# Performance work log

Measured on AMD Instinct MI355X. Metric: run time of the kernel, lower is better.

Reference implementation:

```python
import jax, jax.numpy as jnp
import numpy as np

NUM_HEADS = 8
NUM_GROUPS = 32
EPS = 1e-5


def setup_inputs() -> dict:
    key = jax.random.key(0)
    ks = jax.random.split(key, 3)
    B, C, H, W = 8, 512, 32, 32
    X = jax.random.normal(ks[0], (B, C, H, W), dtype=jnp.float32)
    norm_w = jnp.ones((C,), jnp.float32)
    norm_b = jnp.zeros((C,), jnp.float32)
    qkv_w = jax.random.normal(ks[1], (3 * C, C), dtype=jnp.float32) * (1.0 / np.sqrt(C))
    qkv_b = jnp.zeros((3 * C,), jnp.float32)
    proj_w = jax.random.normal(ks[2], (C, C), dtype=jnp.float32) * (1.0 / np.sqrt(C))
    proj_b = jnp.zeros((C,), jnp.float32)
    return {"X": X, "norm_w": norm_w, "norm_b": norm_b,
            "qkv_w": qkv_w, "qkv_b": qkv_b, "proj_w": proj_w, "proj_b": proj_b}


def group_norm(x, w, b):
    B, C, H, W = x.shape
    xg = x.reshape(B, NUM_GROUPS, C // NUM_GROUPS, H, W)
    mean = xg.mean(axis=(2, 3, 4), keepdims=True)
    var = xg.var(axis=(2, 3, 4), keepdims=True)
    xg = (xg - mean) * jax.lax.rsqrt(var + EPS)
    x = xg.reshape(B, C, H, W)
    return x * w[None, :, None, None] + b[None, :, None, None]


def reference(X, norm_w, norm_b, qkv_w, qkv_b, proj_w, proj_b):
    B, C, H, W = X.shape
    hd = C // NUM_HEADS  # head_dim
    residual = X
    Xn = group_norm(X, norm_w, norm_b)
    # 1x1 conv == channel matmul: [B, 3C, H, W]
    qkv = jnp.einsum('oc,bchw->bohw', qkv_w, Xn) + qkv_b[None, :, None, None]
    q, k, v = jnp.split(qkv, 3, axis=1)
    S = H * W
    q = q.reshape(B, NUM_HEADS, hd, S)
    k = k.reshape(B, NUM_HEADS, hd, S)
    v = v.reshape(B, NUM_HEADS, hd, S)
    scale = hd ** -0.5
    attn = jnp.einsum('bhdq,bhdk->bhqk', q, k) * scale  # [B,H,S,S]
    attn = jax.nn.softmax(attn, axis=-1)
    out = jnp.einsum('bhqk,bhdk->bhqd', attn, v)  # [B,H,S,hd]
    out = out.transpose(0, 1, 3, 2).reshape(B, C, H, W)
    out = jnp.einsum('oc,bchw->bohw', proj_w, out) + proj_b[None, :, None, None]
    return out + residual
```

## Files before the change

### kernel.cpp

```cpp
#include <hip/hip_runtime.h>
#include <hip/hip_bf16.h>


#define BATCH 8
#define C 512
#define S 1024
#define HEADS 8
#define OC3 1536

typedef short bf16x8 __attribute__((ext_vector_type(8)));
typedef float f32x4 __attribute__((ext_vector_type(4)));
typedef unsigned u32x2 __attribute__((ext_vector_type(2)));
typedef unsigned short u16;
typedef unsigned short u16x4 __attribute__((ext_vector_type(4)));

__device__ inline short f2bf(float x) {
    union { float f; unsigned u; } v; v.f = x;
    unsigned r = v.u + 0x7fffu + ((v.u >> 16) & 1u);
    return (short)(r >> 16);
}

__device__ inline unsigned cvt_pk_bf16(float lo, float hi) {
    unsigned r;
    asm("v_cvt_pk_bf16_f32 %0, %1, %2" : "=v"(r) : "v"(lo), "v"(hi));
    return r;
}

__device__ inline void gload_lds16(const u16* g, short* l) {
    __builtin_amdgcn_global_load_lds(
        (const __attribute__((address_space(1))) unsigned int*)g,
        (__attribute__((address_space(3))) unsigned int*)l, 16, 0, 0);
}

__global__ __launch_bounds__(512) void prep_kernel(
    const float* __restrict__ X, const float* __restrict__ nw,
    const float* __restrict__ nb, u16* __restrict__ Xn_t,
    const float* __restrict__ wq, const float* __restrict__ wp,
    u16* __restrict__ oq, u16* __restrict__ op)
{
    const int tid = threadIdx.x;
    if (blockIdx.x >= 256) {
        int j = (blockIdx.x - 256) * 512 + tid;
        const float* w; u16* o;
        if (j < 98304) { w = wq; o = oq; }
        else           { w = wp; o = op; j -= 98304; }
        f32x4 a = *(const f32x4*)(w + (size_t)j * 8);
        f32x4 b = *(const f32x4*)(w + (size_t)j * 8 + 4);
        bf16x8 r;
        #pragma unroll
        for (int k = 0; k < 4; ++k) { r[k] = f2bf(a[k]); r[4 + k] = f2bf(b[k]); }
        *(bf16x8*)(o + (size_t)j * 8) = r;
        return;
    }
    const int blk = blockIdx.x;
    const int bi = blk >> 5, g = blk & 31;
    __shared__ __attribute__((aligned(16))) float T[16][1032];
    __shared__ float red[16];
    __shared__ float sh_mr[2];

    const float* Xg = X + ((size_t)bi * C + g * 16) * S;
    float s = 0.f, ss = 0.f;
    #pragma unroll
    for (int r = 0; r < 8; ++r) {
        int idx4 = r * 512 + tid;
        f32x4 v = *(const f32x4*)(Xg + (size_t)idx4 * 4);
        int c = idx4 >> 8, sp = (idx4 * 4) & 1023;
        *(f32x4*)&T[c][sp] = v;
        s  += v[0] + v[1] + v[2] + v[3];
        ss += v[0]*v[0] + v[1]*v[1] + v[2]*v[2] + v[3]*v[3];
    }
    #pragma unroll
    for (int m = 1; m <= 32; m <<= 1) {
        s += __shfl_xor(s, m); ss += __shfl_xor(ss, m);
    }
    if ((tid & 63) == 0) { red[tid >> 6] = s; red[8 + (tid >> 6)] = ss; }
    __syncthreads();
    if (tid == 0) {
        float S1 = 0.f, S2 = 0.f;
        #pragma unroll
        for (int w = 0; w < 8; ++w) { S1 += red[w]; S2 += red[8 + w]; }
        float mean = S1 * (1.f / 16384.f);
        float var  = S2 * (1.f / 16384.f) - mean * mean;
        sh_mr[0] = mean; sh_mr[1] = rsqrtf(var + 1e-5f);
    }
    __syncthreads();
    const float mean = sh_mr[0], rstd = sh_mr[1];
    float rw[16], sb[16];
    #pragma unroll
    for (int c = 0; c < 16; ++c) {
        float w = nw[g * 16 + c], b = nb[g * 16 + c];
        rw[c] = rstd * w;
        sb[c] = b - mean * rw[c];
    }
    #pragma unroll
    for (int r = 0; r < 2; ++r) {
        int sp = r * 512 + tid;
        bf16x8 o0, o1;
        #pragma unroll
        for (int c = 0; c < 8; ++c) o0[c] = f2bf(T[c][sp] * rw[c] + sb[c]);
        #pragma unroll
        for (int c = 0; c < 8; ++c) o1[c] = f2bf(T[8 + c][sp] * rw[8 + c] + sb[8 + c]);
        u16* dst = Xn_t + ((size_t)bi * S + sp) * C + g * 16;
        *(bf16x8*)dst = o0;
        *(bf16x8*)(dst + 8) = o1;
    }
}

__global__ __launch_bounds__(512) void qkv_mfma(
    const u16* __restrict__ A, const u16* __restrict__ Bt,
    const float* __restrict__ bias,
    u16* __restrict__ Qt, u16* __restrict__ Kt, u16* __restrict__ Vn)
{
    const int n0 = blockIdx.x * 256, m0 = blockIdx.y * 256;
    const int bi = blockIdx.z;
    const int tid = threadIdx.x, wave = tid >> 6, lane = tid & 63;
    const int lr = lane & 15, lg = lane >> 4;
    const int wr = wave >> 2, wc = wave & 3;

    __shared__ __attribute__((aligned(16))) short SM[65536];

    f32x4 acc[8][4];
    #pragma unroll
    for (int i = 0; i < 8; ++i)
        #pragma unroll
        for (int j = 0; j < 4; ++j) acc[i][j] = (f32x4){0.f, 0.f, 0.f, 0.f};

    const int l8 = lane >> 3;
    const int c16 = (lane & 7) ^ l8;
    const u16* aBase = A + (size_t)(m0 + wave * 32 + l8) * C + c16 * 8;
    const u16* bBase = Bt + (size_t)bi * S * C + (size_t)(n0 + wave * 32 + l8) * C + c16 * 8;

    auto STAGE = [&](int buf, int t) {
        const int k0 = t * 64;
        short* as = SM + buf * 16384 + wave * 2048;
        short* bs = SM + 32768 + buf * 16384 + wave * 2048;
        #pragma unroll
        for (int j = 0; j < 4; ++j) {
            gload_lds16(aBase + k0 + (size_t)j * 8 * C, as + j * 512);
            gload_lds16(bBase + k0 + (size_t)j * 8 * C, bs + j * 512);
        }
    };

    STAGE(0, 0);
    asm volatile("s_waitcnt vmcnt(0)" ::: "memory");
    __builtin_amdgcn_s_barrier();
    __builtin_amdgcn_sched_barrier(0);

    #pragma unroll
    for (int kt = 0; kt < 8; ++kt) {
        const int cur = kt & 1;
        if (kt < 7) STAGE(cur ^ 1, kt + 1);
        const short* as = SM + cur * 16384;
        const short* bs = SM + 32768 + cur * 16384;

        bf16x8 bfr[4][2];
        #pragma unroll
        for (int nf = 0; nf < 4; ++nf) {
            int r = wc * 64 + nf * 16 + lr;
            #pragma unroll
            for (int h = 0; h < 2; ++h)
                bfr[nf][h] = *(bf16x8*)&bs[r * 64 + (((h << 2) + lg) ^ (r & 7)) * 8];
        }
        #pragma unroll
        for (int half = 0; half < 2; ++half) {
            bf16x8 afr[4][2];
            #pragma unroll
            for (int mf = 0; mf < 4; ++mf) {
                int r = wr * 128 + (half * 4 + mf) * 16 + lr;
                #pragma unroll
                for (int h = 0; h < 2; ++h)
                    afr[mf][h] = *(bf16x8*)&as[r * 64 + (((h << 2) + lg) ^ (r & 7)) * 8];
            }
            __builtin_amdgcn_s_setprio(1);
            #pragma unroll
            for (int mf = 0; mf < 4; ++mf)
                #pragma unroll
                for (int nf = 0; nf < 4; ++nf) {
                    acc[half * 4 + mf][nf] = __builtin_amdgcn_mfma_f32_16x16x32_bf16(
                        afr[mf][0], bfr[nf][0], acc[half * 4 + mf][nf], 0, 0, 0);
                    acc[half * 4 + mf][nf] = __builtin_amdgcn_mfma_f32_16x16x32_bf16(
                        afr[mf][1], bfr[nf][1], acc[half * 4 + mf][nf], 0, 0, 0);
                }
            __builtin_amdgcn_s_setprio(0);
        }
        if (kt < 7) {
            asm volatile("s_waitcnt vmcnt(0)" ::: "memory");
            __builtin_amdgcn_s_barrier();
            __builtin_amdgcn_sched_barrier(0);
        }
    }

    const float QSCALE = 0.125f * 1.44269504088896f;
    if (m0 < 1024) {
        #pragma unroll
        for (int mf = 0; mf < 8; ++mf) {
            const int o3b = m0 + wr * 128 + mf * 16 + 4 * lg;
            float bv[4];
            #pragma unroll
            for (int i = 0; i < 4; ++i) bv[i] = bias[o3b + i];
            #pragma unroll
            for (int nf = 0; nf < 4; ++nf) {
                const int s = n0 + wc * 64 + nf * 16 + lr;
                if (m0 < 512) {
                    int h = o3b >> 6, d = o3b & 63;
                    u16x4 pk;
                    #pragma unroll
                    for (int i = 0; i < 4; ++i)
                        pk[i] = (u16)f2bf((acc[mf][nf][i] + bv[i]) * QSCALE);
                    *(u16x4*)(Qt + (((size_t)bi * 8 + h) * S + s) * 64 + d) = pk;
                } else {
                    int ok = o3b - 512;
                    int h = ok >> 6, d = ok & 63;
                    u16x4 pk;
                    #pragma unroll
                    for (int i = 0; i < 4; ++i) pk[i] = (u16)f2bf(acc[mf][nf][i] + bv[i]);
                    *(u16x4*)(Kt + (((size_t)bi * 8 + h) * S + s) * 64 + d) = pk;
                }
            }
        }
    } else {
        __syncthreads();
        #pragma unroll
        for (int mf = 0; mf < 8; ++mf) {
            const int orl = wr * 128 + mf * 16 + 4 * lg;
            float bv[4];
            #pragma unroll
            for (int i = 0; i < 4; ++i) bv[i] = bias[m0 + orl + i];
            #pragma unroll
            for (int nf = 0; nf < 4; ++nf) {
                const int srl = wc * 64 + nf * 16 + lr;
                #pragma unroll
                for (int i = 0; i < 4; ++i) {
                    int o = orl + i;
                    SM[o * 256 + (srl ^ ((o & 7) << 3))] =
                        (short)f2bf(acc[mf][nf][i] + bv[i]);
                }
            }
        }
        __syncthreads();
        const int o = tid >> 1, half = (tid & 1) * 128;
        const int ov0 = m0 - 1024;
        u16* vdst = Vn + (size_t)(bi * C + ov0 + o) * S + n0 + half;
        #pragma unroll
        for (int c = 0; c < 16; ++c) {
            int sl = half + 8 * c;
            *(bf16x8*)(vdst + 8 * c) = *(bf16x8*)&SM[o * 256 + (sl ^ ((o & 7) << 3))];
        }
    }
}

__global__ __launch_bounds__(256) void attn_mfma(
    const u16* __restrict__ Qt, const u16* __restrict__ Kt,
    const u16* __restrict__ Vn, u16* __restrict__ At)
{
    const int bh = blockIdx.x, qb = blockIdx.y;
    const int bi = bh >> 3, h = bh & 7;
    const int tid = threadIdx.x, wave = tid >> 6, lane = tid & 63;
    const int lr = lane & 15, lg = lane >> 4;
    const int q0 = qb * 128 + wave * 32;

    const u16* qt = Qt + ((size_t)bi * 8 + h) * S * 64;
    const u16* kp = Kt + ((size_t)bi * 8 + h) * S * 64;
    const u16* vp = Vn + (size_t)(bi * C + h * 64) * S;

    __shared__ __attribute__((aligned(16))) short Ks[2][8192];
    __shared__ __attribute__((aligned(16))) short Vs[2][8192];
    __shared__ __attribute__((aligned(16))) unsigned Pw[4][32 * 32];

    bf16x8 bq[2][2];
    #pragma unroll
    for (int qf = 0; qf < 2; ++qf)
        #pragma unroll
        for (int dc = 0; dc < 2; ++dc)
            bq[qf][dc] = *(const bf16x8*)(qt + (size_t)(q0 + qf * 16 + lr) * 64 + dc * 32 + lg * 8);

    float lsum[2] = {0.f, 0.f};
    f32x4 acc[4][2];
    #pragma unroll
    for (int df = 0; df < 4; ++df)
        #pragma unroll
        for (int qf = 0; qf < 2; ++qf) acc[df][qf] = (f32x4){0.f, 0.f, 0.f, 0.f};

    auto STAGE = [&](int buf, int kt0) {
        #pragma unroll
        for (int p = 0; p < 4; ++p) {
            int idx = p * 256 + tid;
            int rk = idx >> 3, sk = (idx & 7) ^ (rk & 7);
            int rv = idx >> 4, sl = idx & 15;
            int sv = ((sl & 7) ^ (rv & 7)) | (sl & 8);
            short* ldsK = &Ks[buf][(p * 256 + (wave << 6)) * 8];
            short* ldsV = &Vs[buf][(p * 256 + (wave << 6)) * 8];
            gload_lds16(kp + (size_t)(kt0 + rk) * 64 + sk * 8, ldsK);
            gload_lds16(vp + (size_t)rv * S + kt0 + sv * 8, ldsV);
        }
    };

    unsigned* pwb = &Pw[wave][0];
    const int swz = (lr & 7) << 2;

    STAGE(0, 0);
    __syncthreads();

    for (int kt = 0; kt < 8; ++kt) {
        const int cur = kt & 1;
        if (kt < 7) STAGE(cur ^ 1, (kt + 1) * 128);

        #pragma unroll
        for (int ck = 0; ck < 2; ++ck) {
            f32x4 sc[4][2];
            __builtin_amdgcn_s_setprio(1);
            #pragma unroll
            for (int kf = 0; kf < 4; ++kf) {
                int rK = ck * 64 + kf * 16 + lr;
                bf16x8 b0 = *(bf16x8*)&Ks[cur][rK * 64 + (lg ^ (rK & 7)) * 8];
                bf16x8 b1 = *(bf16x8*)&Ks[cur][rK * 64 + ((lg + 4) ^ (rK & 7)) * 8];
                #pragma unroll
                for (int qf = 0; qf < 2; ++qf) {
                    f32x4 z = (f32x4){0.f, 0.f, 0.f, 0.f};
                    z = __builtin_amdgcn_mfma_f32_16x16x32_bf16(b0, bq[qf][0], z, 0, 0, 0);
                    sc[kf][qf] = __builtin_amdgcn_mfma_f32_16x16x32_bf16(b1, bq[qf][1], z, 0, 0, 0);
                }
            }
            __builtin_amdgcn_s_setprio(0);

            #pragma unroll
            for (int kf = 0; kf < 4; ++kf)
                #pragma unroll
                for (int qf = 0; qf < 2; ++qf) {
                    float p0 = __builtin_amdgcn_exp2f(sc[kf][qf][0]);
                    float p1 = __builtin_amdgcn_exp2f(sc[kf][qf][1]);
                    float p2 = __builtin_amdgcn_exp2f(sc[kf][qf][2]);
                    float p3 = __builtin_amdgcn_exp2f(sc[kf][qf][3]);
                    lsum[qf] += (p0 + p1) + (p2 + p3);
                    unsigned w0 = cvt_pk_bf16(p0, p1);
                    unsigned w1 = cvt_pk_bf16(p2, p3);
                    int idx = (qf * 16 + lr) * 32 + ((8 * kf + 2 * lg) ^ swz);
                    *(u32x2*)&pwb[idx] = (u32x2){w0, w1};
                }

            bf16x8 pb[2][2];
            #pragma unroll
            for (int qf = 0; qf < 2; ++qf)
                #pragma unroll
                for (int c = 0; c < 2; ++c)
                    pb[qf][c] = *(bf16x8*)&pwb[(qf * 16 + lr) * 32 + ((lg * 4 + 16 * c) ^ swz)];
            __builtin_amdgcn_s_setprio(1);
            #pragma unroll
            for (int df = 0; df < 4; ++df) {
                int rV = df * 16 + lr;
                bf16x8 v0 = *(bf16x8*)&Vs[cur][rV * 128 + (ck * 8 + (lg ^ (rV & 7))) * 8];
                bf16x8 v1 = *(bf16x8*)&Vs[cur][rV * 128 + (ck * 8 + ((lg + 4) ^ (rV & 7))) * 8];
                #pragma unroll
                for (int qf = 0; qf < 2; ++qf) {
                    acc[df][qf] = __builtin_amdgcn_mfma_f32_16x16x32_bf16(v0, pb[qf][0], acc[df][qf], 0, 0, 0);
                    acc[df][qf] = __builtin_amdgcn_mfma_f32_16x16x32_bf16(v1, pb[qf][1], acc[df][qf], 0, 0, 0);
                }
            }
            __builtin_amdgcn_s_setprio(0);
        }
        __syncthreads();
    }

    #pragma unroll
    for (int qf = 0; qf < 2; ++qf) {
        lsum[qf] += __shfl_xor(lsum[qf], 16);
        lsum[qf] += __shfl_xor(lsum[qf], 32);
        float linv = 1.f / lsum[qf];
        #pragma unroll
        for (int df = 0; df < 4; ++df) {
            u16x4 pk;
            #pragma unroll
            for (int i = 0; i < 4; ++i) pk[i] = (u16)f2bf(acc[df][qf][i] * linv);
            *(u16x4*)(At + ((size_t)bi * S + q0 + qf * 16 + lr) * C + h * 64 + df * 16 + 4 * lg) = pk;
        }
    }
}

__global__ __launch_bounds__(256) void proj_mfma(
    const u16* __restrict__ A, const u16* __restrict__ Bt,
    const float* __restrict__ bias, const float* __restrict__ Xres,
    float* __restrict__ out)
{
    const int n0 = blockIdx.x * 128, m0 = blockIdx.y * 128;
    const int bi = blockIdx.z;
    const int tid = threadIdx.x, wave = tid >> 6, lane = tid & 63;
    const int lr = lane & 15, lg = lane >> 4;
    const int wr = wave >> 1, wc = wave & 1;

    __shared__ __attribute__((aligned(16))) short SM[3][8][1024];

    f32x4 acc[4][4];
    #pragma unroll
    for (int i = 0; i < 4; ++i)
        #pragma unroll
        for (int j = 0; j < 4; ++j) acc[i][j] = (f32x4){0.f, 0.f, 0.f, 0.f};

    const u16* aP0 = A + (size_t)(m0 + wave * 16 + lr) * C + lg * 8;
    const u16* aP1 = A + (size_t)(m0 + (wave + 4) * 16 + lr) * C + lg * 8;
    const u16* bP0 = Bt + (size_t)bi * S * C + (size_t)(n0 + wave * 16 + lr) * C + lg * 8;
    const u16* bP1 = Bt + (size_t)bi * S * C + (size_t)(n0 + (wave + 4) * 16 + lr) * C + lg * 8;

    auto STAGE = [&](int buf, int t) {
        const int k0 = t * 32;
        gload_lds16(aP0 + k0, &SM[buf][wave][0]);
        gload_lds16(aP1 + k0, &SM[buf][wave + 4][0]);
        gload_lds16(bP0 + k0, &SM[buf][wave][512]);
        gload_lds16(bP1 + k0, &SM[buf][wave + 4][512]);
    };

    STAGE(0, 0);
    STAGE(1, 1);
    asm volatile("s_waitcnt vmcnt(4)" ::: "memory");
    __builtin_amdgcn_s_barrier();
    __builtin_amdgcn_sched_barrier(0);

    #pragma unroll
    for (int kt = 0; kt < 16; ++kt) {
        const int cur = kt % 3;
        if (kt < 14) STAGE((kt + 2) % 3, kt + 2);
        bf16x8 af[4], bfr[4];
        #pragma unroll
        for (int mf = 0; mf < 4; ++mf) af[mf] = *(bf16x8*)&SM[cur][wr * 4 + mf][lane * 8];
        #pragma unroll
        for (int nf = 0; nf < 4; ++nf) bfr[nf] = *(bf16x8*)&SM[cur][wc * 4 + nf][512 + lane * 8];
        __builtin_amdgcn_s_setprio(1);
        #pragma unroll
        for (int mf = 0; mf < 4; ++mf)
            #pragma unroll
            for (int nf = 0; nf < 4; ++nf)
                acc[mf][nf] = __builtin_amdgcn_mfma_f32_16x16x32_bf16(
                    af[mf], bfr[nf], acc[mf][nf], 0, 0, 0);
        __builtin_amdgcn_s_setprio(0);
        if (kt < 15) {
            if (kt < 14) asm volatile("s_waitcnt vmcnt(4)" ::: "memory");
            else         asm volatile("s_waitcnt vmcnt(0)" ::: "memory");
            __builtin_amdgcn_s_barrier();
            __builtin_amdgcn_sched_barrier(0);
        }
    }

    #pragma unroll
    for (int mf = 0; mf < 4; ++mf) {
        const int ob = m0 + wr * 64 + mf * 16 + 4 * lg;
        float bv[4];
        #pragma unroll
        for (int i = 0; i < 4; ++i) bv[i] = bias[ob + i];
        #pragma unroll
        for (int nf = 0; nf < 4; ++nf) {
            const int s = n0 + wc * 64 + nf * 16 + lr;
            #pragma unroll
            for (int i = 0; i < 4; ++i) {
                size_t oi = ((size_t)bi * C + ob + i) * S + s;
                out[oi] = acc[mf][nf][i] + bv[i] + Xres[oi];
            }
        }
    }
}

extern "C" void kernel_launch(void* const* d_in, const int* in_sizes, int n_in,
                              void* d_out, int out_size, void* d_ws, size_t ws_size,
                              hipStream_t stream) {
    const float* X      = (const float*)d_in[0];
    const float* norm_w = (const float*)d_in[1];
    const float* norm_b = (const float*)d_in[2];
    const float* qkv_w  = (const float*)d_in[3];
    const float* qkv_b  = (const float*)d_in[4];
    const float* proj_w = (const float*)d_in[5];
    const float* proj_b = (const float*)d_in[6];
    float* out = (float*)d_out;

    u16* Wq_bf = (u16*)d_ws;
    u16* Wp_bf = Wq_bf + 786432;
    u16* Xn_t  = Wp_bf + 262144;
    u16* Qt    = Xn_t + 4194304;
    u16* Kt    = Qt + 4194304;
    u16* Vn    = Kt + 4194304;
    u16* At    = Vn + 4194304;

    prep_kernel<<<dim3(512), 512, 0, stream>>>(
        X, norm_w, norm_b, Xn_t, qkv_w, proj_w, Wq_bf, Wp_bf);
    qkv_mfma<<<dim3(S / 256, OC3 / 256, BATCH), 512, 0, stream>>>(
        Wq_bf, Xn_t, qkv_b, Qt, Kt, Vn);
    attn_mfma<<<dim3(64, S / 128), 256, 0, stream>>>(Qt, Kt, Vn, At);
    proj_mfma<<<dim3(S / 128, C / 128, BATCH), 256, 0, stream>>>(
        Wp_bf, At, proj_b, X, out);
}
```

Before: 75.98 us.

## Interleave global-to-LDS prefetch with MFMA phases in QKV GEMM main loop

Splits the K-loop body of the QKV projection GEMM into four phases of two M-fragments each. The next tile's A and B global-to-LDS loads are issued separately in the first two phases instead of all at the top. Block barriers around each MFMA phase keep waves in lockstep, a ping-pong style schedule meant to overlap memory issue with tensor-core work. The extra barriers per k-step add synchronisation cost and may reduce latency hiding across waves.

```diff
diff --git a/kernel.cpp b/kernel.cpp
--- a/kernel.cpp
+++ b/kernel.cpp
@@ -130,18 +130,21 @@
     const u16* aBase = A + (size_t)(m0 + wave * 32 + l8) * C + c16 * 8;
     const u16* bBase = Bt + (size_t)bi * S * C + (size_t)(n0 + wave * 32 + l8) * C + c16 * 8;
 
-    auto STAGE = [&](int buf, int t) {
-        const int k0 = t * 64;
+    auto STAGE_A = [&](int buf, int t) {
         short* as = SM + buf * 16384 + wave * 2048;
+        #pragma unroll
+        for (int j = 0; j < 4; ++j)
+            gload_lds16(aBase + t * 64 + (size_t)j * 8 * C, as + j * 512);
+    };
+    auto STAGE_B = [&](int buf, int t) {
         short* bs = SM + 32768 + buf * 16384 + wave * 2048;
         #pragma unroll
-        for (int j = 0; j < 4; ++j) {
-            gload_lds16(aBase + k0 + (size_t)j * 8 * C, as + j * 512);
-            gload_lds16(bBase + k0 + (size_t)j * 8 * C, bs + j * 512);
-        }
+        for (int j = 0; j < 4; ++j)
+            gload_lds16(bBase + t * 64 + (size_t)j * 8 * C, bs + j * 512);
     };
 
-    STAGE(0, 0);
+    STAGE_A(0, 0);
+    STAGE_B(0, 0);
     asm volatile("s_waitcnt vmcnt(0)" ::: "memory");
     __builtin_amdgcn_s_barrier();
     __builtin_amdgcn_sched_barrier(0);
@@ -149,7 +152,6 @@
     #pragma unroll
     for (int kt = 0; kt < 8; ++kt) {
         const int cur = kt & 1;
-        if (kt < 7) STAGE(cur ^ 1, kt + 1);
         const short* as = SM + cur * 16384;
         const short* bs = SM + 32768 + cur * 16384;
 
@@ -157,32 +159,40 @@
         #pragma unroll
         for (int nf = 0; nf < 4; ++nf) {
             int r = wc * 64 + nf * 16 + lr;
-            #pragma unroll
-            for (int h = 0; h < 2; ++h)
-                bfr[nf][h] = *(bf16x8*)&bs[r * 64 + (((h << 2) + lg) ^ (r & 7)) * 8];
-        }
-        #pragma unroll
-        for (int half = 0; half < 2; ++half) {
-            bf16x8 afr[4][2];
-            #pragma unroll
-            for (int mf = 0; mf < 4; ++mf) {
-                int r = wr * 128 + (half * 4 + mf) * 16 + lr;
-                #pragma unroll
-                for (int h = 0; h < 2; ++h)
-                    afr[mf][h] = *(bf16x8*)&as[r * 64 + (((h << 2) + lg) ^ (r & 7)) * 8];
-            }
+            bfr[nf][0] = *(bf16x8*)&bs[r * 64 + ((lg) ^ (r & 7)) * 8];
+            bfr[nf][1] = *(bf16x8*)&bs[r * 64 + ((4 + lg) ^ (r & 7)) * 8];
+        }
+
+        #pragma unroll
+        for (int p = 0; p < 4; ++p) {
+            bf16x8 afr[2][2];
+            #pragma unroll
+            for (int m2 = 0; m2 < 2; ++m2) {
+                int r = wr * 128 + (2 * p + m2) * 16 + lr;
+                afr[m2][0] = *(bf16x8*)&as[r * 64 + ((lg) ^ (r & 7)) * 8];
+                afr[m2][1] = *(bf16x8*)&as[r * 64 + ((4 + lg) ^ (r & 7)) * 8];
+            }
+            if (kt < 7) {
+                if (p == 0) STAGE_A(cur ^ 1, kt + 1);
+                else if (p == 1) STAGE_B(cur ^ 1, kt + 1);
+            }
+            __builtin_amdgcn_s_barrier();
             __builtin_amdgcn_s_setprio(1);
             #pragma unroll
-            for (int mf = 0; mf < 4; ++mf)
+            for (int m2 = 0; m2 < 2; ++m2) {
+                int mf = 2 * p + m2;
                 #pragma unroll
                 for (int nf = 0; nf < 4; ++nf) {
-                    acc[half * 4 + mf][nf] = __builtin_amdgcn_mfma_f32_16x16x32_bf16(
-                        afr[mf][0], bfr[nf][0], acc[half * 4 + mf][nf], 0, 0, 0);
-                    acc[half * 4 + mf][nf] = __builtin_amdgcn_mfma_f32_16x16x32_bf16(
-                        afr[mf][1], bfr[nf][1], acc[half * 4 + mf][nf], 0, 0, 0);
-                }
+                    acc[mf][nf] = __builtin_amdgcn_mfma_f32_16x16x32_bf16(
+                        afr[m2][0], bfr[nf][0], acc[mf][nf], 0, 0, 0);
+                    acc[mf][nf] = __builtin_amdgcn_mfma_f32_16x16x32_bf16(
+                        afr[m2][1], bfr[nf][1], acc[mf][nf], 0, 0, 0);
+                }
+            }
             __builtin_amdgcn_s_setprio(0);
-        }
+            __builtin_amdgcn_s_barrier();
+        }
+
         if (kt < 7) {
             asm volatile("s_waitcnt vmcnt(0)" ::: "memory");
             __builtin_amdgcn_s_barrier();
```

Measured after the change: 77.49 us. No clear change (+2.0%).
